# Kernel optimization log

Measured on AMD Instinct MI355X. Metric: run time of the kernel, lower is better.

Reference implementation:

```python
import jax, jax.numpy as jnp
import numpy as np
from jax import lax

B, C, N = 128, 320, 256
H = W = 16
GROUPS = 5
RATIO = 8
MASK_EPS = 1e-6   # registered buffer 'eps' in the torch module
GN_EPS = 1e-5     # torch GroupNorm default


def setup_inputs() -> dict:
    key = jax.random.key(0)
    ks = jax.random.split(key, 10)
    def rn(k, shape, scale=0.05):
        return jax.random.normal(k, shape, dtype=jnp.float32) * scale
    return {
        "x": jax.random.normal(ks[0], (B, C, N), dtype=jnp.float32),
        "low_cutoff": jnp.float32(0.2),
        "high_cutoff": jnp.float32(0.7),
        "ca_w1": rn(ks[1], (C // RATIO, C)),
        "ca_b1": jnp.zeros((C // RATIO,), jnp.float32),
        "ca_w2": rn(ks[2], (3 * C, C // RATIO)),
        "ca_b2": jnp.zeros((3 * C,), jnp.float32),
        "low_w": rn(ks[3], (C, C, 3, 3)),
        "low_b": jnp.zeros((C,), jnp.float32),
        "low_g": jnp.ones((C,), jnp.float32),
        "low_beta": jnp.zeros((C,), jnp.float32),
        "mid_w": rn(ks[4], (C, C, 3, 3)),
        "mid_b": jnp.zeros((C,), jnp.float32),
        "mid_g": jnp.ones((C,), jnp.float32),
        "mid_beta": jnp.zeros((C,), jnp.float32),
        "high_w": rn(ks[5], (C, C, 3, 3)),
        "high_b": jnp.zeros((C,), jnp.float32),
        "high_g": jnp.ones((C,), jnp.float32),
        "high_beta": jnp.zeros((C,), jnp.float32),
        "sa_w": rn(ks[6], (1, C, 1, 1)),
        "sa_b": jnp.zeros((1,), jnp.float32),
    }


def _conv3x3_gn(y, w, b, gamma, beta):
    # Conv2d(C,C,3,padding=1) -> GroupNorm(5,C)
    out = lax.conv_general_dilated(
        y, w, window_strides=(1, 1), padding='SAME',
        dimension_numbers=('NCHW', 'OIHW', 'NCHW'))
    out = out + b[None, :, None, None]
    b_, c_, h_, w_ = out.shape
    g = out.reshape(b_, GROUPS, c_ // GROUPS, h_, w_)
    mu = g.mean(axis=(2, 3, 4), keepdims=True)
    var = g.var(axis=(2, 3, 4), keepdims=True)
    g = (g - mu) * lax.rsqrt(var + GN_EPS)
    out = g.reshape(b_, c_, h_, w_)
    return out * gamma[None, :, None, None] + beta[None, :, None, None]


def reference(x, low_cutoff, high_cutoff, ca_w1, ca_b1, ca_w2, ca_b2,
              low_w, low_b, low_g, low_beta,
              mid_w, mid_b, mid_g, mid_beta,
              high_w, high_b, high_g, high_beta,
              sa_w, sa_b):
    b, c, n = x.shape
    n_pix = H * W
    # reshape_to_square (N == n_pix here, pad/slice kept for faithfulness)
    if n < n_pix:
        xp = jnp.pad(x, ((0, 0), (0, 0), (0, n_pix - n)))
    else:
        xp = x[:, :, :n_pix]
    x2d = xp.reshape(b, c, H, W)

    # DynamicFrequencyFilter: avgpool over N -> 1x1 conv1d -> relu -> 1x1 conv1d -> sigmoid
    avg = x.mean(axis=-1)                                  # [B, C]
    hcw = jax.nn.relu(avg @ ca_w1.T + ca_b1)               # [B, C//8]
    cw = jax.nn.sigmoid(hcw @ ca_w2.T + ca_b2)             # [B, 3C]
    cw = cw.reshape(b, 3, c, 1, 1)

    # FFT + shifted frequency masks. torch fftshift(dim=None) shifts all dims,
    # but the B/C shifts commute with the (B/C-broadcast) mask multiply and are
    # undone by ifftshift, so shifting only the spatial axes is equivalent.
    fft_feat = jnp.fft.fftshift(jnp.fft.fft2(x2d), axes=(-2, -1))
    yy, xx = jnp.meshgrid(jnp.linspace(-1.0, 1.0, H), jnp.linspace(-1.0, 1.0, W), indexing='ij')
    dist = jnp.sqrt(xx ** 2 + yy ** 2) / np.sqrt(2.0)
    low_mask = jax.nn.sigmoid((low_cutoff - dist) / MASK_EPS)
    mid_mask = jax.nn.sigmoid((dist - low_cutoff) / MASK_EPS) * jax.nn.sigmoid((high_cutoff - dist) / MASK_EPS)
    high_mask = jax.nn.sigmoid((dist - high_cutoff) / MASK_EPS)

    def band(mask):
        return jnp.fft.ifft2(jnp.fft.ifftshift(fft_feat * mask, axes=(-2, -1))).real

    low_feat = _conv3x3_gn(band(low_mask), low_w, low_b, low_g, low_beta) + x2d
    mid_feat = _conv3x3_gn(band(mid_mask), mid_w, mid_b, mid_g, mid_beta) + x2d
    high_feat = _conv3x3_gn(band(high_mask), high_w, high_b, high_g, high_beta) + x2d

    fused = cw[:, 0] * low_feat + cw[:, 1] * mid_feat + cw[:, 2] * high_feat

    # spatial attention: 1x1 conv C->1, sigmoid
    sw = jax.nn.sigmoid(jnp.einsum('bchw,c->bhw', fused, sa_w[0, :, 0, 0])[:, None] + sa_b[0])
    out = (fused * sw).reshape(b, c, n_pix)
    return out[:, :, :n]
```

## Files before the change

kernel.cpp:

```cpp
#include <hip/hip_runtime.h>
#include <math.h>

#define NB 128
#define NC 320
#define NG 5
#define CPG 64
#define NHID 40

typedef short bf16x8 __attribute__((ext_vector_type(8)));
typedef short s16x4  __attribute__((ext_vector_type(4)));
typedef float f32x4  __attribute__((ext_vector_type(4)));

__device__ __forceinline__ float sigf(float x){ return 1.0f/(1.0f+expf(-x)); }

__device__ __forceinline__ unsigned short f2b(float f){
  unsigned u = __float_as_uint(f);
  unsigned r = (u + 0x7fffu + ((u >> 16) & 1u)) >> 16;
  return (unsigned short)r;
}
__device__ __forceinline__ float b2f(unsigned short u){
  return __uint_as_float(((unsigned)u) << 16);
}

__device__ __forceinline__ void gll16(const void* g, void* l){
  __builtin_amdgcn_global_load_lds(
      (const __attribute__((address_space(1))) void*)g,
      (__attribute__((address_space(3))) void*)l, 16, 0, 0);
}

__global__ __launch_bounds__(256) void k_prep(const float* __restrict__ lowc,
                                              const float* __restrict__ highc,
                                              const float* __restrict__ w0,
                                              const float* __restrict__ w1,
                                              const float* __restrict__ w2,
                                              unsigned short* __restrict__ WgT,
                                              unsigned short* __restrict__ WAb){
  __shared__ float msh[256];
  __shared__ float cost[16];
  __shared__ float ksh[256];
  __shared__ float wsh[2880];
  int bid = blockIdx.x, t = threadIdx.x;

  if (bid < 768){
    int band = bid >> 8, p = bid & 255;
    float lc = lowc[0], hc = highc[0];
    {
      int a1 = t >> 4, a2 = t & 15;
      const float step = 2.0f / 15.0f;
      float cy = -1.0f + step * (float)a1;
      float cx = -1.0f + step * (float)a2;
      float dist = sqrtf(cx*cx + cy*cy) / 1.41421356237309515f;
      float m = band == 0 ? sigf((lc - dist) * 1e6f)
              : band == 1 ? sigf((dist - lc) * 1e6f) * sigf((hc - dist) * 1e6f)
                          : sigf((dist - hc) * 1e6f);
      msh[t] = m;
    }
    if (t < 16) cost[t] = cosf((float)t * 0.392699081698724154f);
    __syncthreads();
    {
      int d1 = t >> 4, d2 = t & 15;
      float s = 0.f;
      int ang0 = (8*d1 + 8*d2) & 15;
      for (int a1 = 0; a1 < 16; ++a1){
        int ang = (ang0 + a1*d1) & 15;
        #pragma unroll
        for (int a2 = 0; a2 < 16; ++a2){
          s += msh[a1*16 + a2] * cost[ang];
          ang = (ang + d2) & 15;
        }
      }
      ksh[t] = s * (1.0f/256.0f);
    }
    __syncthreads();
    int d1 = ((p >> 4) - (t >> 4)) & 15;
    int d2 = ((p & 15) - (t & 15)) & 15;
    WgT[(size_t)(band << 16) + (p << 8) + t] = f2b(ksh[(d1 << 4) | d2]);
  } else {
    int bid2 = bid - 768;
    int band = bid2 / 320, co = bid2 % 320;
    const float* w = band == 0 ? w0 : (band == 1 ? w1 : w2);
    const float* src = w + (size_t)co * 2880;
    for (int i = t; i < 2880; i += 256) wsh[i] = src[i];
    __syncthreads();
    unsigned short* dst = WAb + (size_t)band * 921600;
    for (int g = t; g < 360; g += 256){
      int tap = g / 40, r = g % 40;
      unsigned short tmp[8];
      #pragma unroll
      for (int j = 0; j < 8; ++j) tmp[j] = f2b(wsh[(r*8 + j)*9 + tap]);
      s16x4* o = (s16x4*)(dst + (size_t)g * 2560 + co*8);
      o[0] = *(s16x4*)tmp;
      o[1] = *(s16x4*)(tmp + 4);
    }
  }
}

__global__ __launch_bounds__(256, 4) void k_bandg3(const float* __restrict__ x,
                                                   const unsigned short* __restrict__ WgT,
                                                   unsigned short* __restrict__ bandT,
                                                   float* __restrict__ avgOut){
  __shared__ unsigned short xt[64*256];
  int tid = threadIdx.x;
  int wgid = (blockIdx.x & 7)*80 + (blockIdx.x >> 3);
  int b = wgid / 5, cq = wgid % 5;
  int cibase = cq * 64;
  size_t rowbase = (size_t)wgid * 64;

  {
    int r = tid >> 2, c0 = (tid & 3) * 64;
    const float* xp = x + (rowbase + r)*256 + c0;
    unsigned short* dp = xt + r*256;
    int sw = (r & 7) << 3;
    float rs = 0.f;
    #pragma unroll
    for (int j = 0; j < 64; j += 4){
      float4 f = *(const float4*)(xp + j);
      rs += f.x + f.y + f.z + f.w;
      unsigned short t4[4] = { f2b(f.x), f2b(f.y), f2b(f.z), f2b(f.w) };
      *(s16x4*)(dp + ((c0 + j) ^ sw)) = *(s16x4*)t4;
    }
    rs += __shfl_down(rs, 1);
    rs += __shfl_down(rs, 2);
    if ((tid & 3) == 0) avgOut[rowbase + r] = rs * (1.0f/256.0f);
  }

  for (int i = tid; i < 3264; i += 256){
    int band = i / 1088, r = i % 1088;
    int si = r >> 4, cg = r & 15;
    int rr, cc;
    if (si < 18)      { rr = 0;        cc = si;      }
    else if (si < 36) { rr = 17;       cc = si - 18; }
    else if (si < 52) { rr = si - 35;  cc = 0;       }
    else              { rr = si - 51;  cc = 17;      }
    s16x4 z = {0,0,0,0};
    *(s16x4*)(bandT + (size_t)band*13271040 +
              ((size_t)(b*324 + rr*18 + cc))*NC + cibase + cg*4) = z;
  }
  __syncthreads();

  int l  = tid & 63;
  int wq = tid >> 6;
  int cig = l >> 4, lan = l & 15;

  for (int band = 0; band < 3; ++band){
    const unsigned short* Wg = WgT + (size_t)band * 65536;
    unsigned short* bT = bandT + (size_t)band * 13271040;

    f32x4 acc[4][4];
    #pragma unroll
    for (int m = 0; m < 4; ++m)
      #pragma unroll
      for (int n = 0; n < 4; ++n) acc[m][n] = (f32x4){0.f,0.f,0.f,0.f};

    #pragma unroll 2
    for (int ks = 0; ks < 8; ++ks){
      int koff = ks*32 + cig*8;
      bf16x8 a[4], bv[4];
      #pragma unroll
      for (int m = 0; m < 4; ++m){
        int row = m*16 + lan;
        a[m] = *(const bf16x8*)(xt + row*256 + (koff ^ ((row & 7) << 3)));
      }
      #pragma unroll
      for (int n = 0; n < 4; ++n){
        int p = wq*64 + n*16 + lan;
        bv[n] = *(const bf16x8*)(Wg + (size_t)p*256 + koff);
      }
      #pragma unroll
      for (int m = 0; m < 4; ++m)
        #pragma unroll
        for (int n = 0; n < 4; ++n)
          acc[m][n] = __builtin_amdgcn_mfma_f32_16x16x32_bf16(a[m], bv[n], acc[m][n], 0, 0, 0);
    }

    #pragma unroll
    for (int m = 0; m < 4; ++m){
      #pragma unroll
      for (int n = 0; n < 4; ++n){
        int p = wq*64 + n*16 + lan;
        int slot = ((p >> 4) + 1) * 18 + (p & 15) + 1;
        int ci = cibase + m*16 + cig*4;
        unsigned short o[4] = { f2b(acc[m][n][0]), f2b(acc[m][n][1]),
                                f2b(acc[m][n][2]), f2b(acc[m][n][3]) };
        *(s16x4*)(bT + ((size_t)(b*324 + slot))*NC + ci) = *(s16x4*)o;
      }
    }
  }
}

__global__ __launch_bounds__(256, 3) void k_convg(const unsigned short* __restrict__ bandT,
                                                  const unsigned short* __restrict__ WAb,
                                                  const float* __restrict__ bias0,
                                                  const float* __restrict__ bias1,
                                                  const float* __restrict__ bias2,
                                                  unsigned short* __restrict__ convb,
                                                  float* __restrict__ stats_part){
  __shared__ char ldsA[3*10240];
  __shared__ char ldsB[2*11520];
  __shared__ float stw[4][5][2];

  int tid = threadIdx.x;
  int wgid = (blockIdx.x & 7)*192 + (blockIdx.x >> 3);
  int band = wgid / 512; int rem = wgid & 511;
  int b = rem >> 2, ch = (rem >> 1) & 1, ph = rem & 1;

  const unsigned short* bT = bandT + (size_t)band*13271040 + (size_t)b*103680;
  const unsigned short* WA = WAb + (size_t)band*921600;
  const float* bias = band == 0 ? bias0 : (band == 1 ? bias1 : bias2);
  unsigned short* cbp = convb + (size_t)band * 10485760;

  int l = tid & 63, w = tid >> 6;
  int wco = w >> 1, wpx = w & 1;
  int cig = l >> 4, lan = l & 15;
  int cobase = ch*160 + wco*80;
  int px0 = ph*128 + wpx*64;

  int ga0 = tid, ga1 = tid + 256, ga2 = tid + 512;
  int aoff0 = (ga0/160)*2560 + (ga0%160)*8 + ch*1280;
  int aoff1 = (ga1/160)*2560 + (ga1%160)*8 + ch*1280;
  int aoff2 = (ga2/160)*2560 + (ga2%160)*8 + ch*1280;
  int gb0 = tid, gb1 = tid + 256, gb2 = tid + 512;
  int boff0 = (ph*144 + gb0%180)*320 + (gb0/180)*8;
  int boff1 = (ph*144 + gb1%180)*320 + (gb1/180)*8;
  int boff2 = (ph*144 + gb2%180)*320 + (gb2/180)*8;

  int Aread0 = (cig*160 + wco*80 + lan)*16;
  int Bread0 = (cig*180 + (wpx*4 + 1)*18 + lan + 1)*16;

  f32x4 acc[5][4];
  #pragma unroll
  for (int m = 0; m < 5; ++m)
    #pragma unroll
    for (int n = 0; n < 4; ++n) acc[m][n] = (f32x4){0.f,0.f,0.f,0.f};

#define STAGE_A(TAP, CIB, BUF) do { \
    const unsigned short* sA = WA + (size_t)((TAP)*40 + (CIB)*4)*2560; \
    char* dA = ldsA + (BUF)*10240; \
    gll16(sA + aoff0, dA + tid*16); \
    gll16(sA + aoff1, dA + 4096 + tid*16); \
    if (tid < 128) gll16(sA + aoff2, dA + 8192 + tid*16); \
  } while(0)

#define STAGE_B(CN) do { \
    const unsigned short* sB = bT + (CN)*32; \
    char* dB = ldsB + ((CN)&1)*11520; \
    gll16(sB + boff0, dB + tid*16); \
    gll16(sB + boff1, dB + 4096 + tid*16); \
    if (tid < 208) gll16(sB + boff2, dB + 8192 + tid*16); \
  } while(0)

#define VWAIT(N) asm volatile("s_waitcnt vmcnt(" #N ")" ::: "memory")

  STAGE_A(0, 0, 0);
  STAGE_B(0);
  STAGE_A(1, 0, 1);
  VWAIT(2);
  __builtin_amdgcn_s_barrier();

  for (int cib = 0; cib < 10; ++cib){
    #pragma unroll
    for (int tap = 0; tap < 9; ++tap){
      const char* Ab = ldsA + (tap % 3)*10240 + Aread0;
      bf16x8 a0 = *(const bf16x8*)(Ab);
      bf16x8 a1 = *(const bf16x8*)(Ab + 256);
      bf16x8 a2 = *(const bf16x8*)(Ab + 512);
      bf16x8 a3 = *(const bf16x8*)(Ab + 768);
      bf16x8 a4 = *(const bf16x8*)(Ab + 1024);
      const int dhdw = ((tap/3)*18 + (tap%3) - 19)*16;
      const char* Bb = ldsB + (cib & 1)*11520 + Bread0 + dhdw;
      bf16x8 b0 = *(const bf16x8*)(Bb);
      bf16x8 b1 = *(const bf16x8*)(Bb + 288);
      bf16x8 b2 = *(const bf16x8*)(Bb + 576);
      bf16x8 b3 = *(const bf16x8*)(Bb + 864);

      if (tap <= 6){
        STAGE_A(tap + 2, cib, (tap + 2) % 3);
      } else if (cib < 9){
        STAGE_A(tap - 7, cib + 1, (tap + 2) % 3);
      }
      if (tap == 0 && cib < 9) STAGE_B(cib + 1);

      __builtin_amdgcn_s_setprio(1);
      acc[0][0] = __builtin_amdgcn_mfma_f32_16x16x32_bf16(a0, b0, acc[0][0],0,0,0);
      acc[0][1] = __builtin_amdgcn_mfma_f32_16x16x32_bf16(a0, b1, acc[0][1],0,0,0);
      acc[0][2] = __builtin_amdgcn_mfma_f32_16x16x32_bf16(a0, b2, acc[0][2],0,0,0);
      acc[0][3] = __builtin_amdgcn_mfma_f32_16x16x32_bf16(a0, b3, acc[0][3],0,0,0);
      acc[1][0] = __builtin_amdgcn_mfma_f32_16x16x32_bf16(a1, b0, acc[1][0],0,0,0);
      acc[1][1] = __builtin_amdgcn_mfma_f32_16x16x32_bf16(a1, b1, acc[1][1],0,0,0);
      acc[1][2] = __builtin_amdgcn_mfma_f32_16x16x32_bf16(a1, b2, acc[1][2],0,0,0);
      acc[1][3] = __builtin_amdgcn_mfma_f32_16x16x32_bf16(a1, b3, acc[1][3],0,0,0);
      acc[2][0] = __builtin_amdgcn_mfma_f32_16x16x32_bf16(a2, b0, acc[2][0],0,0,0);
      acc[2][1] = __builtin_amdgcn_mfma_f32_16x16x32_bf16(a2, b1, acc[2][1],0,0,0);
      acc[2][2] = __builtin_amdgcn_mfma_f32_16x16x32_bf16(a2, b2, acc[2][2],0,0,0);
      acc[2][3] = __builtin_amdgcn_mfma_f32_16x16x32_bf16(a2, b3, acc[2][3],0,0,0);
      acc[3][0] = __builtin_amdgcn_mfma_f32_16x16x32_bf16(a3, b0, acc[3][0],0,0,0);
      acc[3][1] = __builtin_amdgcn_mfma_f32_16x16x32_bf16(a3, b1, acc[3][1],0,0,0);
      acc[3][2] = __builtin_amdgcn_mfma_f32_16x16x32_bf16(a3, b2, acc[3][2],0,0,0);
      acc[3][3] = __builtin_amdgcn_mfma_f32_16x16x32_bf16(a3, b3, acc[3][3],0,0,0);
      acc[4][0] = __builtin_amdgcn_mfma_f32_16x16x32_bf16(a4, b0, acc[4][0],0,0,0);
      acc[4][1] = __builtin_amdgcn_mfma_f32_16x16x32_bf16(a4, b1, acc[4][1],0,0,0);
      acc[4][2] = __builtin_amdgcn_mfma_f32_16x16x32_bf16(a4, b2, acc[4][2],0,0,0);
      acc[4][3] = __builtin_amdgcn_mfma_f32_16x16x32_bf16(a4, b3, acc[4][3],0,0,0);
      __builtin_amdgcn_s_setprio(0);

      if (tap <= 1){
        if (cib < 9) { VWAIT(5); } else { VWAIT(2); }
      } else if (tap == 7){
        if (cib < 9) { VWAIT(2); } else { VWAIT(0); }
      } else if (tap == 8){
        if (cib < 9) { VWAIT(2); }
      } else {
        VWAIT(2);
      }
      if (!(cib == 9 && tap == 8)) __builtin_amdgcn_s_barrier();
    }
  }
#undef STAGE_A
#undef STAGE_B
#undef VWAIT

  #pragma unroll
  for (int m = 0; m < 5; ++m)
    #pragma unroll
    for (int r = 0; r < 4; ++r){
      float bvs = bias[cobase + m*16 + cig*4 + r];
      #pragma unroll
      for (int n = 0; n < 4; ++n) acc[m][n][r] += bvs;
    }

  #pragma unroll
  for (int m = 0; m < 5; ++m){
    float s = 0.f, q = 0.f;
    #pragma unroll
    for (int n = 0; n < 4; ++n)
      #pragma unroll
      for (int r = 0; r < 4; ++r){ float v = acc[m][n][r]; s += v; q += v*v; }
    #pragma unroll
    for (int o = 32; o > 0; o >>= 1){ s += __shfl_xor(s, o); q += __shfl_xor(q, o); }
    if (l == 0){ stw[w][m][0] = s; stw[w][m][1] = q; }
  }

  #pragma unroll
  for (int m = 0; m < 5; ++m)
    #pragma unroll
    for (int r = 0; r < 4; ++r){
      int co = cobase + m*16 + cig*4 + r;
      unsigned short* op = cbp + ((size_t)(b*NC + co))*256 + px0 + lan;
      #pragma unroll
      for (int n = 0; n < 4; ++n) op[n*16] = f2b(acc[m][n][r]);
    }

  __syncthreads();
  if (tid < 6){
    int gl = tid >> 1, comp = tid & 1;
    int g = ch*2 + gl;
    float t = 0.f;
    for (int w2 = 0; w2 < 4; ++w2)
      #pragma unroll
      for (int m = 0; m < 5; ++m)
        if (((ch*160 + (w2 >> 1)*80 + m*16) >> 6) == g) t += stw[w2][m][comp];
    stats_part[((size_t)(band*NB + b)*NG + g)*8 + ch*4 + ph*2 + comp] = t;
  }
}

__global__ __launch_bounds__(512) void k_fuse3(const unsigned short* __restrict__ cb0,
                                               const unsigned short* __restrict__ cb1,
                                               const unsigned short* __restrict__ cb2,
                                               const float* __restrict__ x,
                                               const float* __restrict__ stats_part,
                                               const float* __restrict__ g0, const float* __restrict__ be0,
                                               const float* __restrict__ g1, const float* __restrict__ be1,
                                               const float* __restrict__ g2, const float* __restrict__ be2,
                                               const float* __restrict__ avg,
                                               const float* __restrict__ caw1,
                                               const float* __restrict__ cab1,
                                               const float* __restrict__ caw2,
                                               const float* __restrict__ cab2,
                                               const float* __restrict__ saw,
                                               const float* __restrict__ sab,
                                               float* __restrict__ out){
  __shared__ unsigned short fl[NC*128];
  __shared__ float mu_s[3][NG], rs_s[3][NG], sh[4][128];
  __shared__ float avs[NC], hsh[NHID], cws[3*NC];
  int b = blockIdx.x >> 1, half = blockIdx.x & 1;
  int tid = threadIdx.x;

  if (tid < NC) avs[tid] = avg[b*NC + tid];
  else if (tid >= 496 && tid < 511){
    int t2 = tid - 496;
    int band = t2 / 5, g = t2 % 5;
    const float* sp = stats_part + ((size_t)(band*NB + b)*NG + g)*8;
    float s = 0.f, q = 0.f;
    if (g <= 2){ s += sp[0] + sp[2]; q += sp[1] + sp[3]; }
    if (g >= 2){ s += sp[4] + sp[6]; q += sp[5] + sp[7]; }
    float mu = s * (1.f/16384.f);
    float var = q * (1.f/16384.f) - mu*mu;
    mu_s[band][g] = mu; rs_s[band][g] = rsqrtf(var + 1e-5f);
  }
  __syncthreads();
  if (tid < NHID){
    float s = cab1[tid];
    const float* wr = caw1 + tid*NC;
    for (int i = 0; i < NC; ++i) s += wr[i] * avs[i];
    hsh[tid] = fmaxf(s, 0.0f);
  }
  __syncthreads();
  for (int o = tid; o < 3*NC; o += 512){
    float s = cab2[o];
    const float* wr = caw2 + o*NHID;
    #pragma unroll
    for (int i = 0; i < NHID; ++i) s += wr[i] * hsh[i];
    cws[o] = sigf(s);
  }
  __syncthreads();

  int p = tid & 127, cs = tid >> 7;
  int px = half*128 + p;
  float sacc = 0.f;
  for (int ci = cs; ci < NC; ci += 4){
    int g = ci >> 6;
    size_t idx = ((size_t)(b*NC + ci))*256 + px;
    float xv = x[idx];
    float f =
      cws[ci      ] * ((b2f(cb0[idx]) - mu_s[0][g])*rs_s[0][g]*g0[ci] + be0[ci] + xv) +
      cws[320 + ci] * ((b2f(cb1[idx]) - mu_s[1][g])*rs_s[1][g]*g1[ci] + be1[ci] + xv) +
      cws[640 + ci] * ((b2f(cb2[idx]) - mu_s[2][g])*rs_s[2][g]*g2[ci] + be2[ci] + xv);
    fl[ci*128 + p] = f2b(f);
    sacc += f * saw[ci];
  }
  sh[cs][p] = sacc;
  __syncthreads();
  if (tid < 128) sh[0][tid] = sigf(sh[0][tid] + sh[1][tid] + sh[2][tid] + sh[3][tid] + sab[0]);
  __syncthreads();
  float swv = sh[0][p];
  for (int ci = cs; ci < NC; ci += 4){
    size_t idx = ((size_t)(b*NC + ci))*256 + px;
    out[idx] = b2f(fl[ci*128 + p]) * swv;
  }
}

extern "C" void kernel_launch(void* const* d_in, const int* in_sizes, int n_in,
                              void* d_out, int out_size, void* d_ws, size_t ws_size,
                              hipStream_t stream){
  (void)in_sizes; (void)n_in; (void)out_size; (void)ws_size;
  const float* x     = (const float*)d_in[0];
  const float* lowc  = (const float*)d_in[1];
  const float* highc = (const float*)d_in[2];
  const float* ca_w1 = (const float*)d_in[3];
  const float* ca_b1 = (const float*)d_in[4];
  const float* ca_w2 = (const float*)d_in[5];
  const float* ca_b2 = (const float*)d_in[6];
  const float* conv_w[3] = {(const float*)d_in[7],  (const float*)d_in[11], (const float*)d_in[15]};
  const float* conv_b[3] = {(const float*)d_in[8],  (const float*)d_in[12], (const float*)d_in[16]};
  const float* gn_g[3]   = {(const float*)d_in[9],  (const float*)d_in[13], (const float*)d_in[17]};
  const float* gn_be[3]  = {(const float*)d_in[10], (const float*)d_in[14], (const float*)d_in[18]};
  const float* sa_w = (const float*)d_in[19];
  const float* sa_b = (const float*)d_in[20];
  float* out = (float*)d_out;

  char* base = (char*)d_ws;
  unsigned short* WgT   = (unsigned short*)(base + 4096);
  unsigned short* WAb   = (unsigned short*)(base + 397312);
  unsigned short* bandT = (unsigned short*)(base + 5926912);
  unsigned short* cbb   = (unsigned short*)(base + 85553152);
  float*          avg   = (float*)(base + 148959232);
  float*          stats = (float*)(base + 149123072);
  unsigned short* cb0 = cbb;
  unsigned short* cb1 = cbb + 10485760;
  unsigned short* cb2 = cbb + 20971520;

  k_prep  <<<1728, 256, 0, stream>>>(lowc, highc, conv_w[0], conv_w[1], conv_w[2],
                                     WgT, WAb);

  k_bandg3<<<640, 256, 0, stream>>>(x, WgT, bandT, avg);

  k_convg<<<1536, 256, 0, stream>>>(bandT, WAb, conv_b[0], conv_b[1], conv_b[2],
                                    cbb, stats);

  k_fuse3<<<256, 512, 0, stream>>>(cb0, cb1, cb2, x, stats,
                                   gn_g[0], gn_be[0], gn_g[1], gn_be[1], gn_g[2], gn_be[2],
                                   avg, ca_w1, ca_b1, ca_w2, ca_b2,
                                   sa_w, sa_b, out);
}
```

Measured before the change: 265.2 us.

## Load conv weights directly into registers, bypassing LDS staging

Removes the LDS triple-buffer for the weight (A) operand in the grouped conv kernel. Each wave now loads its A fragments straight from global memory into a pair of register ping-pong buffers, one tap ahead. The input (B) tiles are still double-buffered in LDS, but the loop is restructured to cover two channel blocks per iteration with fewer barriers. This cuts LDS traffic and barrier count for the weights. In exchange it adds redundant global/L2 weight reads across waves, more register pressure, and only one tap of latency hiding for the global loads.

```diff
diff --git a/kernel.cpp b/kernel.cpp
--- a/kernel.cpp
+++ b/kernel.cpp
@@ -195,7 +195,6 @@
                                                   const float* __restrict__ bias2,
                                                   unsigned short* __restrict__ convb,
                                                   float* __restrict__ stats_part){
-  __shared__ char ldsA[3*10240];
   __shared__ char ldsB[2*11520];
   __shared__ float stw[4][5][2];
 
@@ -215,16 +214,13 @@
   int cobase = ch*160 + wco*80;
   int px0 = ph*128 + wpx*64;
 
-  int ga0 = tid, ga1 = tid + 256, ga2 = tid + 512;
-  int aoff0 = (ga0/160)*2560 + (ga0%160)*8 + ch*1280;
-  int aoff1 = (ga1/160)*2560 + (ga1%160)*8 + ch*1280;
-  int aoff2 = (ga2/160)*2560 + (ga2%160)*8 + ch*1280;
+  const unsigned short* Areg = WA + cig*2560 + ch*1280 + (wco*80 + lan)*8;
+
   int gb0 = tid, gb1 = tid + 256, gb2 = tid + 512;
   int boff0 = (ph*144 + gb0%180)*320 + (gb0/180)*8;
   int boff1 = (ph*144 + gb1%180)*320 + (gb1/180)*8;
   int boff2 = (ph*144 + gb2%180)*320 + (gb2/180)*8;
 
-  int Aread0 = (cig*160 + wco*80 + lan)*16;
   int Bread0 = (cig*180 + (wpx*4 + 1)*18 + lan + 1)*16;
 
   f32x4 acc[5][4];
@@ -233,91 +229,86 @@
     #pragma unroll
     for (int n = 0; n < 4; ++n) acc[m][n] = (f32x4){0.f,0.f,0.f,0.f};
 
-#define STAGE_A(TAP, CIB, BUF) do { \
-    const unsigned short* sA = WA + (size_t)((TAP)*40 + (CIB)*4)*2560; \
-    char* dA = ldsA + (BUF)*10240; \
-    gll16(sA + aoff0, dA + tid*16); \
-    gll16(sA + aoff1, dA + 4096 + tid*16); \
-    if (tid < 128) gll16(sA + aoff2, dA + 8192 + tid*16); \
+  bf16x8 A0[5], A1[5];
+
+#define LOADA(ARR, OFS) do { \
+    const unsigned short* p_ = Areg + (OFS); \
+    ARR[0] = *(const bf16x8*)(p_); \
+    ARR[1] = *(const bf16x8*)(p_ + 128); \
+    ARR[2] = *(const bf16x8*)(p_ + 256); \
+    ARR[3] = *(const bf16x8*)(p_ + 384); \
+    ARR[4] = *(const bf16x8*)(p_ + 512); \
   } while(0)
 
-#define STAGE_B(CN) do { \
+#define STAGE_B(CN, BUF) do { \
     const unsigned short* sB = bT + (CN)*32; \
-    char* dB = ldsB + ((CN)&1)*11520; \
+    char* dB = ldsB + (BUF)*11520; \
     gll16(sB + boff0, dB + tid*16); \
     gll16(sB + boff1, dB + 4096 + tid*16); \
     if (tid < 208) gll16(sB + boff2, dB + 8192 + tid*16); \
   } while(0)
 
-#define VWAIT(N) asm volatile("s_waitcnt vmcnt(" #N ")" ::: "memory")
-
-  STAGE_A(0, 0, 0);
-  STAGE_B(0);
-  STAGE_A(1, 0, 1);
-  VWAIT(2);
+  STAGE_B(0, 0);
+  LOADA(A0, 0);
+  asm volatile("s_waitcnt vmcnt(0)" ::: "memory");
   __builtin_amdgcn_s_barrier();
 
-  for (int cib = 0; cib < 10; ++cib){
-    #pragma unroll
-    for (int tap = 0; tap < 9; ++tap){
-      const char* Ab = ldsA + (tap % 3)*10240 + Aread0;
-      bf16x8 a0 = *(const bf16x8*)(Ab);
-      bf16x8 a1 = *(const bf16x8*)(Ab + 256);
-      bf16x8 a2 = *(const bf16x8*)(Ab + 512);
-      bf16x8 a3 = *(const bf16x8*)(Ab + 768);
-      bf16x8 a4 = *(const bf16x8*)(Ab + 1024);
-      const int dhdw = ((tap/3)*18 + (tap%3) - 19)*16;
-      const char* Bb = ldsB + (cib & 1)*11520 + Bread0 + dhdw;
-      bf16x8 b0 = *(const bf16x8*)(Bb);
-      bf16x8 b1 = *(const bf16x8*)(Bb + 288);
-      bf16x8 b2 = *(const bf16x8*)(Bb + 576);
-      bf16x8 b3 = *(const bf16x8*)(Bb + 864);
-
-      if (tap <= 6){
-        STAGE_A(tap + 2, cib, (tap + 2) % 3);
-      } else if (cib < 9){
-        STAGE_A(tap - 7, cib + 1, (tap + 2) % 3);
-      }
-      if (tap == 0 && cib < 9) STAGE_B(cib + 1);
-
-      __builtin_amdgcn_s_setprio(1);
-      acc[0][0] = __builtin_amdgcn_mfma_f32_16x16x32_bf16(a0, b0, acc[0][0],0,0,0);
-      acc[0][1] = __builtin_amdgcn_mfma_f32_16x16x32_bf16(a0, b1, acc[0][1],0,0,0);
-      acc[0][2] = __builtin_amdgcn_mfma_f32_16x16x32_bf16(a0, b2, acc[0][2],0,0,0);
-      acc[0][3] = __builtin_amdgcn_mfma_f32_16x16x32_bf16(a0, b3, acc[0][3],0,0,0);
-      acc[1][0] = __builtin_amdgcn_mfma_f32_16x16x32_bf16(a1, b0, acc[1][0],0,0,0);
-      acc[1][1] = __builtin_amdgcn_mfma_f32_16x16x32_bf16(a1, b1, acc[1][1],0,0,0);
-      acc[1][2] = __builtin_amdgcn_mfma_f32_16x16x32_bf16(a1, b2, acc[1][2],0,0,0);
-      acc[1][3] = __builtin_amdgcn_mfma_f32_16x16x32_bf16(a1, b3, acc[1][3],0,0,0);
-      acc[2][0] = __builtin_amdgcn_mfma_f32_16x16x32_bf16(a2, b0, acc[2][0],0,0,0);
-      acc[2][1] = __builtin_amdgcn_mfma_f32_16x16x32_bf16(a2, b1, acc[2][1],0,0,0);
-      acc[2][2] = __builtin_amdgcn_mfma_f32_16x16x32_bf16(a2, b2, acc[2][2],0,0,0);
-      acc[2][3] = __builtin_amdgcn_mfma_f32_16x16x32_bf16(a2, b3, acc[2][3],0,0,0);
-      acc[3][0] = __builtin_amdgcn_mfma_f32_16x16x32_bf16(a3, b0, acc[3][0],0,0,0);
-      acc[3][1] = __builtin_amdgcn_mfma_f32_16x16x32_bf16(a3, b1, acc[3][1],0,0,0);
-      acc[3][2] = __builtin_amdgcn_mfma_f32_16x16x32_bf16(a3, b2, acc[3][2],0,0,0);
-      acc[3][3] = __builtin_amdgcn_mfma_f32_16x16x32_bf16(a3, b3, acc[3][3],0,0,0);
-      acc[4][0] = __builtin_amdgcn_mfma_f32_16x16x32_bf16(a4, b0, acc[4][0],0,0,0);
-      acc[4][1] = __builtin_amdgcn_mfma_f32_16x16x32_bf16(a4, b1, acc[4][1],0,0,0);
-      acc[4][2] = __builtin_amdgcn_mfma_f32_16x16x32_bf16(a4, b2, acc[4][2],0,0,0);
-      acc[4][3] = __builtin_amdgcn_mfma_f32_16x16x32_bf16(a4, b3, acc[4][3],0,0,0);
-      __builtin_amdgcn_s_setprio(0);
-
-      if (tap <= 1){
-        if (cib < 9) { VWAIT(5); } else { VWAIT(2); }
-      } else if (tap == 7){
-        if (cib < 9) { VWAIT(2); } else { VWAIT(0); }
-      } else if (tap == 8){
-        if (cib < 9) { VWAIT(2); }
-      } else {
-        VWAIT(2);
-      }
-      if (!(cib == 9 && tap == 8)) __builtin_amdgcn_s_barrier();
-    }
-  }
-#undef STAGE_A
+#define BODY(T, CURA, NXTA) do { \
+    if ((T) == 0){ \
+      __builtin_amdgcn_s_barrier(); \
+      STAGE_B(cc2 + 1, 1); \
+    } else if ((T) == 9){ \
+      __builtin_amdgcn_s_barrier(); \
+      if (cib2 < 4) STAGE_B(cc2 + 2, 0); \
+    } \
+    const char* Bb = ldsB + (((T) >= 9) ? 11520 : 0) + Bread0 \
+                   + (((((T)%9)/3)*18 + (((T)%9)%3) - 19)*16); \
+    bf16x8 b0 = *(const bf16x8*)(Bb); \
+    bf16x8 b1 = *(const bf16x8*)(Bb + 288); \
+    bf16x8 b2 = *(const bf16x8*)(Bb + 576); \
+    bf16x8 b3 = *(const bf16x8*)(Bb + 864); \
+    { \
+      size_t ofs_ = ((T) == 17) ? (cc + 20480) \
+          : ((size_t)(((((T)+1)%9))*102400) + cc + ((((T)+1) >= 9) ? 10240 : 0)); \
+      LOADA(NXTA, ofs_); \
+    } \
+    __builtin_amdgcn_s_setprio(1); \
+    acc[0][0]=__builtin_amdgcn_mfma_f32_16x16x32_bf16(CURA[0],b0,acc[0][0],0,0,0); \
+    acc[0][1]=__builtin_amdgcn_mfma_f32_16x16x32_bf16(CURA[0],b1,acc[0][1],0,0,0); \
+    acc[0][2]=__builtin_amdgcn_mfma_f32_16x16x32_bf16(CURA[0],b2,acc[0][2],0,0,0); \
+    acc[0][3]=__builtin_amdgcn_mfma_f32_16x16x32_bf16(CURA[0],b3,acc[0][3],0,0,0); \
+    acc[1][0]=__builtin_amdgcn_mfma_f32_16x16x32_bf16(CURA[1],b0,acc[1][0],0,0,0); \
+    acc[1][1]=__builtin_amdgcn_mfma_f32_16x16x32_bf16(CURA[1],b1,acc[1][1],0,0,0); \
+    acc[1][2]=__builtin_amdgcn_mfma_f32_16x16x32_bf16(CURA[1],b2,acc[1][2],0,0,0); \
+    acc[1][3]=__builtin_amdgcn_mfma_f32_16x16x32_bf16(CURA[1],b3,acc[1][3],0,0,0); \
+    acc[2][0]=__builtin_amdgcn_mfma_f32_16x16x32_bf16(CURA[2],b0,acc[2][0],0,0,0); \
+    acc[2][1]=__builtin_amdgcn_mfma_f32_16x16x32_bf16(CURA[2],b1,acc[2][1],0,0,0); \
+    acc[2][2]=__builtin_amdgcn_mfma_f32_16x16x32_bf16(CURA[2],b2,acc[2][2],0,0,0); \
+    acc[2][3]=__builtin_amdgcn_mfma_f32_16x16x32_bf16(CURA[2],b3,acc[2][3],0,0,0); \
+    acc[3][0]=__builtin_amdgcn_mfma_f32_16x16x32_bf16(CURA[3],b0,acc[3][0],0,0,0); \
+    acc[3][1]=__builtin_amdgcn_mfma_f32_16x16x32_bf16(CURA[3],b1,acc[3][1],0,0,0); \
+    acc[3][2]=__builtin_amdgcn_mfma_f32_16x16x32_bf16(CURA[3],b2,acc[3][2],0,0,0); \
+    acc[3][3]=__builtin_amdgcn_mfma_f32_16x16x32_bf16(CURA[3],b3,acc[3][3],0,0,0); \
+    acc[4][0]=__builtin_amdgcn_mfma_f32_16x16x32_bf16(CURA[4],b0,acc[4][0],0,0,0); \
+    acc[4][1]=__builtin_amdgcn_mfma_f32_16x16x32_bf16(CURA[4],b1,acc[4][1],0,0,0); \
+    acc[4][2]=__builtin_amdgcn_mfma_f32_16x16x32_bf16(CURA[4],b2,acc[4][2],0,0,0); \
+    acc[4][3]=__builtin_amdgcn_mfma_f32_16x16x32_bf16(CURA[4],b3,acc[4][3],0,0,0); \
+    __builtin_amdgcn_s_setprio(0); \
+  } while(0)
+
+  for (int cib2 = 0; cib2 < 5; ++cib2){
+    int cc2 = cib2*2;
+    size_t cc = (size_t)cib2 * 20480;
+    BODY(0,  A0, A1);  BODY(1,  A1, A0);  BODY(2,  A0, A1);
+    BODY(3,  A1, A0);  BODY(4,  A0, A1);  BODY(5,  A1, A0);
+    BODY(6,  A0, A1);  BODY(7,  A1, A0);  BODY(8,  A0, A1);
+    BODY(9,  A1, A0);  BODY(10, A0, A1);  BODY(11, A1, A0);
+    BODY(12, A0, A1);  BODY(13, A1, A0);  BODY(14, A0, A1);
+    BODY(15, A1, A0);  BODY(16, A0, A1);  BODY(17, A1, A0);
+  }
+#undef BODY
 #undef STAGE_B
-#undef VWAIT
+#undef LOADA
 
   #pragma unroll
   for (int m = 0; m < 5; ++m)
```

Result: slower. 281.6 us (+6.2%).
